# Kernel tuning notes

Hardware: AMD Instinct MI355X
Metric: run time of the kernel (lower is better)

## Reference

```python
import jax, jax.numpy as jnp
import numpy as np

B, C_IN, H, W = 4096, 3, 32, 32
C1, C2, K = 32, 64, 3
FC1, NCLS = 256, 10


def _extract_patches(x):
    # x: (B, C, H, W) -> patches (B, C, K*K, H, W), 3x3 neighborhoods, pad=1
    xp = jnp.pad(x, ((0, 0), (0, 0), (1, 1), (1, 1)))
    shifts = [xp[:, :, i:i + H, j:j + W] for i in range(K) for j in range(K)]
    return jnp.stack(shifts, axis=2)


def _maxpool2(x):
    b, c, h, w = x.shape
    return x.reshape(b, c, h // 2, 2, w // 2, 2).max(axis=(3, 5))


def setup_inputs() -> dict:
    key = jax.random.key(0)
    ks = jax.random.split(key, 9)
    # kaiming-ish scales
    s_lc = np.sqrt(2.0 / (C_IN * K * K)).astype(np.float32)
    s_cv = np.sqrt(2.0 / (C1 * K * K)).astype(np.float32)
    s_f1 = np.sqrt(2.0 / (C2 * 8 * 8)).astype(np.float32)
    s_f2 = np.sqrt(2.0 / FC1).astype(np.float32)
    return {
        "x": jax.random.normal(ks[0], (B, C_IN, H, W), dtype=jnp.float32),
        # unshared per-location weights: (O, C, K*K, H, W)
        "w_lc": jax.random.normal(ks[1], (C1, C_IN, K * K, H, W), dtype=jnp.float32) * s_lc,
        "b_lc": jnp.zeros((C1, H, W), dtype=jnp.float32),
        "w_conv": jax.random.normal(ks[2], (C2, C1, K, K), dtype=jnp.float32) * s_cv,
        "b_conv": jnp.zeros((C2,), dtype=jnp.float32),
        "w_fc1": jax.random.normal(ks[3], (FC1, C2 * 8 * 8), dtype=jnp.float32) * s_f1,
        "b_fc1": jnp.zeros((FC1,), dtype=jnp.float32),
        "w_fc2": jax.random.normal(ks[4], (NCLS, FC1), dtype=jnp.float32) * s_f2,
        "b_fc2": jnp.zeros((NCLS,), dtype=jnp.float32),
    }


def reference(x, w_lc, b_lc, w_conv, b_conv, w_fc1, b_fc1, w_fc2, b_fc2):
    # locally connected layer: per-(i,j) unshared 3x3 filters
    patches = _extract_patches(x)                                  # (B, C, 9, H, W)
    y = jnp.einsum('bckij,ockij->boij', patches, w_lc) + b_lc[None]  # (B, C1, H, W)
    y = jax.nn.relu(y)
    y = _maxpool2(y)                                               # (B, C1, 16, 16)
    # standard 3x3 conv, padding SAME
    y = jax.lax.conv_general_dilated(
        y, w_conv, window_strides=(1, 1), padding='SAME',
        dimension_numbers=('NCHW', 'OIHW', 'NCHW'))
    y = jax.nn.relu(y + b_conv[None, :, None, None])
    y = _maxpool2(y)                                               # (B, C2, 8, 8)
    y = y.reshape(y.shape[0], -1)                                  # (B, C2*8*8)
    y = jax.nn.relu(y @ w_fc1.T + b_fc1)
    return y @ w_fc2.T + b_fc2                                     # (B, num_classes)
```

## Files before the change

kernel.cpp:

```cpp
#include <hip/hip_runtime.h>

typedef short s16x8 __attribute__((ext_vector_type(8)));
typedef float f32x4 __attribute__((ext_vector_type(4)));
typedef unsigned short u16x4 __attribute__((ext_vector_type(4)));

static __device__ __forceinline__ unsigned short f2bf(float f) {
    union { float f; unsigned u; } v; v.f = f;
    unsigned r = v.u + 0x7FFF + ((v.u >> 16) & 1);
    return (unsigned short)(r >> 16);
}
static __device__ __forceinline__ float quad_fmax(float a) {
    int ai = __builtin_bit_cast(int, a);
    int s1 = __builtin_amdgcn_mov_dpp(ai, 0xB1, 0xF, 0xF, true);
    a = fmaxf(a, __builtin_bit_cast(float, s1));
    ai = __builtin_bit_cast(int, a);
    int s2 = __builtin_amdgcn_mov_dpp(ai, 0x4E, 0xF, 0xF, true);
    return fmaxf(a, __builtin_bit_cast(float, s2));
}

__global__ __launch_bounds__(256) void k_prep(
    const float* __restrict__ w_lc, const float* __restrict__ b_lc,
    const float* __restrict__ w_conv, const float* __restrict__ w_fc1,
    unsigned short* __restrict__ btab, unsigned short* __restrict__ wt_g,
    unsigned short* __restrict__ Wb)
{
    const int t = threadIdx.x, bx = blockIdx.x;
    if (bx < 1024) {
        const int gid = bx * 256 + t;
        const int k8 = gid & 7;
        const int nn = (gid >> 3) & 127;
        const int jp = (gid >> 10) & 15;
        const int pr = gid >> 14;
        const int o = nn >> 2, ih = (nn >> 1) & 1, jc = nn & 1;
        const int row = 2 * pr + ih, col = 2 * jp + jc;
        unsigned v32[8];
        #pragma unroll
        for (int e = 0; e < 8; ++e) {
            const int k = k8 * 8 + e;
            float v = 0.f;
            if (k < 48) {
                const int c = k >> 4, rr = (k >> 2) & 3, cf = k & 3;
                const int di = rr - ih, dj = cf - jc;
                if ((unsigned)di < 3u && (unsigned)dj < 3u)
                    v = w_lc[((o * 3 + c) * 9 + di * 3 + dj) * 1024 + row * 32 + col];
            } else if (k == 63) {
                v = b_lc[o * 1024 + row * 32 + col];
            }
            v32[e] = f2bf(v);
        }
        uint4 w;
        w.x = v32[0] | (v32[1] << 16);
        w.y = v32[2] | (v32[3] << 16);
        w.z = v32[4] | (v32[5] << 16);
        w.w = v32[6] | (v32[7] << 16);
        *(uint4*)&btab[(size_t)gid * 8] = w;
    } else if (bx < 1088) {
        const float4* wf4 = (const float4*)w_fc1;
        for (int f = t; f < 4096; f += 256) {
            const int idx = (bx - 1024) * 4096 + f;
            const float4 v = wf4[idx];
            u16x4 o = { f2bf(v.x), f2bf(v.y), f2bf(v.z), f2bf(v.w) };
            *(u16x4*)&Wb[idx * 4] = o;
        }
    } else {
        for (int i = t; i < 9 * 64 * 40; i += 256) wt_g[i] = 0;
        __syncthreads();
        for (int i = t; i < 64 * 32 * 9; i += 256) {
            const int oc = i / 288;
            const int rem = i - oc * 288;
            const int ic = rem / 9;
            const int kk = rem - ic * 9;
            wt_g[(kk * 64 + oc) * 40 + ic] = f2bf(w_conv[i]);
        }
    }
}

__global__ __launch_bounds__(256, 4) void k_lc(
    const float* __restrict__ x,
    const unsigned short* __restrict__ btab,
    unsigned short* __restrict__ y1g)
{
    __shared__ unsigned short xb_raw[8 + 12 * 33 * 34 + 8];
    __shared__ __align__(16) unsigned short pbuf[2][32][40];
    const int t = threadIdx.x;
    const int ib = blockIdx.x >> 4;
    const int pr = blockIdx.x & 15;
    const int img0 = ib * 32;
    unsigned short* xbp = xb_raw + 8;

    for (int f = t; f < (8 + 12 * 33 * 34 + 8) / 2; f += 256) ((int*)xb_raw)[f] = 0;
    __syncthreads();
    #pragma unroll
    for (int i = 0; i < 12; ++i) {
        const int f = t + i * 256;
        const int img = f / 96;
        const int rem = f - img * 96;
        const int c = rem >> 5, rr = (rem >> 3) & 3, cf = rem & 7;
        const int xrow = 2 * pr - 1 + rr;
        if ((unsigned)xrow < 32u) {
            const float4 v = *(const float4*)&x[
                ((size_t)(img0 + img) * 3 + c) * 1024 + xrow * 32 + cf * 4];
            const unsigned w0 = (unsigned)f2bf(v.x) | ((unsigned)f2bf(v.y) << 16);
            const unsigned w1 = (unsigned)f2bf(v.z) | ((unsigned)f2bf(v.w) << 16);
            const int imgl = (img & 15) + (img >> 4) * 17;
            const int sa = ((c * 4 + rr) * 33 + imgl) * 34 + cf * 4;
            *(unsigned*)&xbp[sa] = w0;
            *(unsigned*)&xbp[sa + 2] = w1;
        }
    }
    __syncthreads();

    const int lane = t & 63, wv = t >> 6;
    const int lc = lane & 15, lg = lane >> 4;
    const unsigned short* bpb = btab + (((size_t)pr * 16) * 128 + wv * 32) * 64;

    const int r1a = (8 + lg * 2 > 11) ? 11 : 8 + lg * 2;
    const int r1b = (9 + lg * 2 > 11) ? 11 : 9 + lg * 2;

#define LOADB(B, jpv)                                                          \
    {                                                                          \
        const unsigned short* bp = bpb + (size_t)(jpv) * (128 * 64);           \
        B[0] = *(const s16x8*)&bp[lc * 64 + lg * 8];                           \
        B[1] = *(const s16x8*)&bp[(16 + lc) * 64 + lg * 8];                    \
        B[2] = *(const s16x8*)&bp[lc * 64 + 32 + lg * 8];                      \
        B[3] = *(const s16x8*)&bp[(16 + lc) * 64 + 32 + lg * 8];               \
    }

#define ABUILD(wout, row0, row1, mbase, colb2, biasfix)                        \
    {                                                                          \
        const int rows_[2] = { row0, row1 };                                   \
        _Pragma("unroll")                                                      \
        for (int rI = 0; rI < 2; ++rI) {                                       \
            const int base = (rows_[rI] * 33 + (mbase)) * 34 + (colb2);        \
            const unsigned d0 = *(const unsigned*)&xbp[base];                  \
            const unsigned d1 = *(const unsigned*)&xbp[base + 2];              \
            const unsigned d2 = *(const unsigned*)&xbp[base + 4];              \
            wout[rI * 2 + 0] = (unsigned)(((((unsigned long long)d1) << 32) | d0) >> 16); \
            wout[rI * 2 + 1] = (unsigned)(((((unsigned long long)d2) << 32) | d1) >> 16); \
        }                                                                      \
        if (biasfix && lg == 3) wout[3] = 0x3F800000u;                         \
    }

#define STEP(jpv, B)                                                           \
    {                                                                          \
        const int colb2 = (jpv) * 2 - 2;                                       \
        f32x4 acc[2][2];                                                       \
        _Pragma("unroll")                                                      \
        for (int mh = 0; mh < 2; ++mh)                                         \
            _Pragma("unroll")                                                  \
            for (int nf = 0; nf < 2; ++nf) {                                   \
                f32x4 z = {0.f, 0.f, 0.f, 0.f};                                \
                acc[mh][nf] = z;                                               \
            }                                                                  \
        _Pragma("unroll")                                                      \
        for (int mh = 0; mh < 2; ++mh) {                                       \
            const int mbase = mh * 17 + lc;                                    \
            unsigned wa[4], wb[4];                                             \
            ABUILD(wa, lg * 2, lg * 2 + 1, mbase, colb2, 0)                    \
            ABUILD(wb, r1a, r1b, mbase, colb2, 1)                              \
            uint4 ai = { wa[0], wa[1], wa[2], wa[3] };                         \
            uint4 bi = { wb[0], wb[1], wb[2], wb[3] };                         \
            const s16x8 a0 = __builtin_bit_cast(s16x8, ai);                    \
            const s16x8 a1 = __builtin_bit_cast(s16x8, bi);                    \
            acc[mh][0] = __builtin_amdgcn_mfma_f32_16x16x32_bf16(a0, B[0], acc[mh][0], 0, 0, 0); \
            acc[mh][1] = __builtin_amdgcn_mfma_f32_16x16x32_bf16(a0, B[1], acc[mh][1], 0, 0, 0); \
            acc[mh][0] = __builtin_amdgcn_mfma_f32_16x16x32_bf16(a1, B[2], acc[mh][0], 0, 0, 0); \
            acc[mh][1] = __builtin_amdgcn_mfma_f32_16x16x32_bf16(a1, B[3], acc[mh][1], 0, 0, 0); \
        }                                                                      \
        _Pragma("unroll")                                                      \
        for (int mh = 0; mh < 2; ++mh)                                         \
            _Pragma("unroll")                                                  \
            for (int nf = 0; nf < 2; ++nf) {                                   \
                f32x4 v = acc[mh][nf];                                         \
                _Pragma("unroll")                                              \
                for (int q = 0; q < 4; ++q) v[q] = quad_fmax(v[q]);            \
                const float sel = (lc & 2) ? ((lc & 1) ? v[3] : v[2])          \
                                           : ((lc & 1) ? v[1] : v[0]);         \
                const float m = fmaxf(sel, 0.f);                               \
                pbuf[(jpv) & 1][mh * 16 + lg * 4 + (lc & 3)]                   \
                    [wv * 8 + nf * 4 + (lc >> 2)] = f2bf(m);                   \
            }                                                                  \
    }

    s16x8 Ba[4], Bb[4];
    LOADB(Ba, 0)
    for (int jp2 = 0; jp2 < 8; ++jp2) {
        LOADB(Bb, (jp2 * 2 + 1) & 15)
        STEP(jp2 * 2, Ba)
        LOADB(Ba, (jp2 * 2 + 2) & 15)
        STEP(jp2 * 2 + 1, Bb)
        {
            const int img = lane >> 1, jpq = lane & 1;
            const int jpg = jp2 * 2 + jpq;
            *(s16x8*)&y1g[(((size_t)(img0 + img) * 256) + pr * 16 + jpg) * 32 + wv * 8] =
                *(const s16x8*)&pbuf[jpq][img][wv * 8];
        }
    }
#undef STEP
#undef ABUILD
#undef LOADB
}

__global__ __launch_bounds__(256, 3) void k_conv(
    const unsigned short* __restrict__ y1g,
    const unsigned short* __restrict__ wt_g,
    const float* __restrict__ b_conv,
    unsigned short* __restrict__ p2)
{
    __shared__ __align__(16) unsigned short y1t[18][18][40];
    __shared__ __align__(16) unsigned short pbuf[4][1024];
    const int t = threadIdx.x;
    const int img = blockIdx.x;

    {
        const s16x8 z = {0, 0, 0, 0, 0, 0, 0, 0};
        unsigned short* p = &y1t[0][0][0];
        for (int i = t * 8; i < 18 * 18 * 40; i += 2048) *(s16x8*)(p + i) = z;
    }
    __syncthreads();
    {
        const int prr = t >> 4, pcc = t & 15;
        const unsigned short* src = y1g + ((size_t)img * 256 + t) * 32;
        unsigned short* d = &y1t[prr + 1][pcc + 1][0];
        #pragma unroll
        for (int ch = 0; ch < 4; ++ch)
            *(s16x8*)(d + ch * 8) = *(const s16x8*)(src + ch * 8);
    }
    __syncthreads();

    const int w = t >> 6, lane = t & 63;
    const int lc = lane & 15, lg = lane >> 4;

    f32x4 acc[4][4];
    #pragma unroll
    for (int mf = 0; mf < 4; ++mf)
        #pragma unroll
        for (int nf = 0; nf < 4; ++nf) {
            f32x4 zz = {0.f, 0.f, 0.f, 0.f};
            acc[mf][nf] = zz;
        }
    #pragma unroll
    for (int kk = 0; kk < 9; ++kk) {
        const int di = kk / 3, dj = kk % 3;
        s16x8 a[4], bb[4];
        #pragma unroll
        for (int nf = 0; nf < 4; ++nf)
            bb[nf] = *(const s16x8*)&wt_g[(kk * 64 + nf * 16 + lc) * 40 + lg * 8];
        #pragma unroll
        for (int mf = 0; mf < 4; ++mf)
            a[mf] = *(const s16x8*)&y1t[w * 4 + mf + di][lc + dj][lg * 8];
        #pragma unroll
        for (int mf = 0; mf < 4; ++mf)
            #pragma unroll
            for (int nf = 0; nf < 4; ++nf)
                acc[mf][nf] = __builtin_amdgcn_mfma_f32_16x16x32_bf16(
                    a[mf], bb[nf], acc[mf][nf], 0, 0, 0);
    }
    #pragma unroll
    for (int mfp = 0; mfp < 2; ++mfp) {
        #pragma unroll
        for (int nf = 0; nf < 4; ++nf) {
            const f32x4 u = acc[mfp * 2][nf], v = acc[mfp * 2 + 1][nf];
            const float bbv = b_conv[nf * 16 + lc];
            float q0 = fmaxf(fmaxf(u[0], u[1]), fmaxf(v[0], v[1]));
            float q1 = fmaxf(fmaxf(u[2], u[3]), fmaxf(v[2], v[3]));
            q0 = fmaxf(q0 + bbv, 0.f);
            q1 = fmaxf(q1 + bbv, 0.f);
            *(unsigned*)&pbuf[w][(nf * 16 + lc) * 16 + mfp * 8 + lg * 2] =
                (unsigned)f2bf(q0) | ((unsigned)f2bf(q1) << 16);
        }
    }
    #pragma unroll
    for (int jj = 0; jj < 2; ++jj) {
        const int u8 = jj * 64 + lane;
        const int oc = u8 >> 1, s = (u8 & 1) * 8;
        const s16x8 val = *(const s16x8*)&pbuf[w][u8 * 8];
        *(s16x8*)&p2[((size_t)img * 64 + oc) * 64 + w * 16 + s] = val;
    }
}

__global__ __launch_bounds__(256) void k_fc1(
    const unsigned short* __restrict__ A,
    const unsigned short* __restrict__ Wb,
    const float* __restrict__ bias, float* __restrict__ fc1p)
{
    __shared__ __align__(16) unsigned short As[64][72];
    __shared__ __align__(16) unsigned short Bs[32][72];
    const int t = threadIdx.x;
    const int m0 = blockIdx.x * 64, n0 = blockIdx.y * 32;
    const int z = blockIdx.z;
    const int w = t >> 6, lane = t & 63;
    const int lc = lane & 15, lg = lane >> 4;
    f32x4 acc[2];
    {
        const float bv0 = (z == 0) ? bias[n0 + lc] : 0.f;
        const float bv1 = (z == 0) ? bias[n0 + 16 + lc] : 0.f;
        f32x4 a0 = {bv0, bv0, bv0, bv0}, a1 = {bv1, bv1, bv1, bv1};
        acc[0] = a0; acc[1] = a1;
    }
    const int kbase = z * 2048;
    for (int k0 = kbase; k0 < kbase + 2048; k0 += 64) {
        {
            const int r0 = t >> 3, ch0 = (t & 7) * 8;
            const int id1 = t + 256;
            const int r1 = id1 >> 3, ch1 = (id1 & 7) * 8;
            *(s16x8*)&As[r0][ch0] = *(const s16x8*)&A[(size_t)(m0 + r0) * 4096 + k0 + ch0];
            *(s16x8*)&As[r1][ch1] = *(const s16x8*)&A[(size_t)(m0 + r1) * 4096 + k0 + ch1];
            const int rb = t >> 3, cb = (t & 7) * 8;
            *(s16x8*)&Bs[rb][cb] = *(const s16x8*)&Wb[(size_t)(n0 + rb) * 4096 + k0 + cb];
        }
        __syncthreads();
        #pragma unroll
        for (int kh = 0; kh < 2; ++kh) {
            const s16x8 a  = *(const s16x8*)&As[w * 16 + lc][kh * 32 + lg * 8];
            const s16x8 b0 = *(const s16x8*)&Bs[lc][kh * 32 + lg * 8];
            const s16x8 b1 = *(const s16x8*)&Bs[16 + lc][kh * 32 + lg * 8];
            acc[0] = __builtin_amdgcn_mfma_f32_16x16x32_bf16(a, b0, acc[0], 0, 0, 0);
            acc[1] = __builtin_amdgcn_mfma_f32_16x16x32_bf16(a, b1, acc[1], 0, 0, 0);
        }
        __syncthreads();
    }
    #pragma unroll
    for (int nf = 0; nf < 2; ++nf) {
        const int n = n0 + nf * 16 + lc;
        #pragma unroll
        for (int q = 0; q < 4; ++q) {
            const int m = m0 + w * 16 + lg * 4 + q;
            fc1p[((size_t)z * 4096 + m) * 256 + n] = acc[nf][q];
        }
    }
}

__global__ __launch_bounds__(320) void k_fc2(
    const float* __restrict__ fc1p, const float* __restrict__ Wt,
    const float* __restrict__ bias, float* __restrict__ out)
{
    const int t = threadIdx.x;
    const int r = blockIdx.x * 32 + t / 10;
    const int n = t % 10;
    const float4* a0 = (const float4*)(fc1p + (size_t)r * 256);
    const float4* a1 = (const float4*)(fc1p + (size_t)(4096 + r) * 256);
    const float4* w = (const float4*)(Wt + (size_t)n * 256);
    float acc = bias[n];
    #pragma unroll 8
    for (int k = 0; k < 64; ++k) {
        const float4 u = a0[k], v = a1[k], wv = w[k];
        acc += fmaxf(u.x + v.x, 0.f) * wv.x + fmaxf(u.y + v.y, 0.f) * wv.y +
               fmaxf(u.z + v.z, 0.f) * wv.z + fmaxf(u.w + v.w, 0.f) * wv.w;
    }
    out[(size_t)r * 10 + n] = acc;
}

extern "C" void kernel_launch(void* const* d_in, const int* in_sizes, int n_in,
                              void* d_out, int out_size, void* d_ws, size_t ws_size,
                              hipStream_t stream)
{
    const float* x      = (const float*)d_in[0];
    const float* w_lc   = (const float*)d_in[1];
    const float* b_lc   = (const float*)d_in[2];
    const float* w_conv = (const float*)d_in[3];
    const float* b_conv = (const float*)d_in[4];
    const float* w_fc1  = (const float*)d_in[5];
    const float* b_fc1  = (const float*)d_in[6];
    const float* w_fc2  = (const float*)d_in[7];
    const float* b_fc2  = (const float*)d_in[8];
    float* out = (float*)d_out;

    unsigned short* p2b  = (unsigned short*)d_ws;
    unsigned short* btab = (unsigned short*)((char*)d_ws + 16777216);
    unsigned short* y1g  = (unsigned short*)((char*)d_ws + 33554432);
    float*          fc1p = (float*)((char*)d_ws + 33554432);
    unsigned short* Wb   = (unsigned short*)((char*)d_ws + 67108864);
    unsigned short* wt_g = (unsigned short*)((char*)d_ws + 69206016);

    k_prep<<<1089, 256, 0, stream>>>(w_lc, b_lc, w_conv, w_fc1, btab, wt_g, Wb);
    for (int half = 0; half < 2; ++half) {
        k_lc<<<1024, 256, 0, stream>>>(x + (size_t)half * 2048 * 3072, btab, y1g);
        k_conv<<<2048, 256, 0, stream>>>(y1g, wt_g, b_conv,
                                         p2b + (size_t)half * 2048 * 4096);
    }
    k_fc1<<<dim3(64, 8, 2), 256, 0, stream>>>(p2b, Wb, b_fc1, fc1p);
    k_fc2<<<128, 320, 0, stream>>>(fc1p, w_fc2, b_fc2, out);
}
```

Baseline: 200.3 us.

## Halve images per locally-connected block to raise occupancy and simplify loop

Each k_lc block now processes 16 images instead of 32, and the grid doubles to 2048 blocks. This halves the shared-memory input tile and pooled buffer, and the launch bound allows 8 blocks per CU instead of 4. The explicit double-buffered prefetch of the B fragments is replaced by a plain per-column loop with one M-tile. Each wave now stores its pooled outputs directly from a single buffer through its first 16 lanes. In exchange, per-location weights are reloaded twice as often across the grid, and without the software prefetch the compiler must hide the load latency.

```diff
diff --git a/kernel.cpp b/kernel.cpp
--- a/kernel.cpp
+++ b/kernel.cpp
@@ -75,23 +75,23 @@
     }
 }
 
-__global__ __launch_bounds__(256, 4) void k_lc(
+__global__ __launch_bounds__(256, 8) void k_lc(
     const float* __restrict__ x,
     const unsigned short* __restrict__ btab,
     unsigned short* __restrict__ y1g)
 {
-    __shared__ unsigned short xb_raw[8 + 12 * 33 * 34 + 8];
-    __shared__ __align__(16) unsigned short pbuf[2][32][40];
+    __shared__ unsigned short xb_raw[8 + 12 * 17 * 34 + 8];
+    __shared__ __align__(16) unsigned short pbuf[16][40];
     const int t = threadIdx.x;
     const int ib = blockIdx.x >> 4;
     const int pr = blockIdx.x & 15;
-    const int img0 = ib * 32;
+    const int img0 = ib * 16;
     unsigned short* xbp = xb_raw + 8;
 
-    for (int f = t; f < (8 + 12 * 33 * 34 + 8) / 2; f += 256) ((int*)xb_raw)[f] = 0;
+    for (int f = t; f < (8 + 12 * 17 * 34 + 8) / 2; f += 256) ((int*)xb_raw)[f] = 0;
     __syncthreads();
     #pragma unroll
-    for (int i = 0; i < 12; ++i) {
+    for (int i = 0; i < 6; ++i) {
         const int f = t + i * 256;
         const int img = f / 96;
         const int rem = f - img * 96;
@@ -102,8 +102,7 @@
                 ((size_t)(img0 + img) * 3 + c) * 1024 + xrow * 32 + cf * 4];
             const unsigned w0 = (unsigned)f2bf(v.x) | ((unsigned)f2bf(v.y) << 16);
             const unsigned w1 = (unsigned)f2bf(v.z) | ((unsigned)f2bf(v.w) << 16);
-            const int imgl = (img & 15) + (img >> 4) * 17;
-            const int sa = ((c * 4 + rr) * 33 + imgl) * 34 + cf * 4;
+            const int sa = ((c * 4 + rr) * 17 + img) * 34 + cf * 4;
             *(unsigned*)&xbp[sa] = w0;
             *(unsigned*)&xbp[sa + 2] = w1;
         }
@@ -117,21 +116,14 @@
     const int r1a = (8 + lg * 2 > 11) ? 11 : 8 + lg * 2;
     const int r1b = (9 + lg * 2 > 11) ? 11 : 9 + lg * 2;
 
-#define LOADB(B, jpv)                                                          \
-    {                                                                          \
-        const unsigned short* bp = bpb + (size_t)(jpv) * (128 * 64);           \
-        B[0] = *(const s16x8*)&bp[lc * 64 + lg * 8];                           \
-        B[1] = *(const s16x8*)&bp[(16 + lc) * 64 + lg * 8];                    \
-        B[2] = *(const s16x8*)&bp[lc * 64 + 32 + lg * 8];                      \
-        B[3] = *(const s16x8*)&bp[(16 + lc) * 64 + 32 + lg * 8];               \
-    }
-
-#define ABUILD(wout, row0, row1, mbase, colb2, biasfix)                        \
+    unsigned short* ybase = y1g + (((size_t)(img0 + lc) * 256) + pr * 16) * 32 + wv * 8;
+
+#define ABUILD(wout, row0, row1, colb2, biasfix)                               \
     {                                                                          \
         const int rows_[2] = { row0, row1 };                                   \
         _Pragma("unroll")                                                      \
         for (int rI = 0; rI < 2; ++rI) {                                       \
-            const int base = (rows_[rI] * 33 + (mbase)) * 34 + (colb2);        \
+            const int base = (rows_[rI] * 17 + lc) * 34 + (colb2);             \
             const unsigned d0 = *(const unsigned*)&xbp[base];                  \
             const unsigned d1 = *(const unsigned*)&xbp[base + 2];              \
             const unsigned d2 = *(const unsigned*)&xbp[base + 4];              \
@@ -141,64 +133,47 @@
         if (biasfix && lg == 3) wout[3] = 0x3F800000u;                         \
     }
 
-#define STEP(jpv, B)                                                           \
-    {                                                                          \
-        const int colb2 = (jpv) * 2 - 2;                                       \
-        f32x4 acc[2][2];                                                       \
-        _Pragma("unroll")                                                      \
-        for (int mh = 0; mh < 2; ++mh)                                         \
-            _Pragma("unroll")                                                  \
-            for (int nf = 0; nf < 2; ++nf) {                                   \
-                f32x4 z = {0.f, 0.f, 0.f, 0.f};                                \
-                acc[mh][nf] = z;                                               \
-            }                                                                  \
-        _Pragma("unroll")                                                      \
-        for (int mh = 0; mh < 2; ++mh) {                                       \
-            const int mbase = mh * 17 + lc;                                    \
-            unsigned wa[4], wb[4];                                             \
-            ABUILD(wa, lg * 2, lg * 2 + 1, mbase, colb2, 0)                    \
-            ABUILD(wb, r1a, r1b, mbase, colb2, 1)                              \
-            uint4 ai = { wa[0], wa[1], wa[2], wa[3] };                         \
-            uint4 bi = { wb[0], wb[1], wb[2], wb[3] };                         \
-            const s16x8 a0 = __builtin_bit_cast(s16x8, ai);                    \
-            const s16x8 a1 = __builtin_bit_cast(s16x8, bi);                    \
-            acc[mh][0] = __builtin_amdgcn_mfma_f32_16x16x32_bf16(a0, B[0], acc[mh][0], 0, 0, 0); \
-            acc[mh][1] = __builtin_amdgcn_mfma_f32_16x16x32_bf16(a0, B[1], acc[mh][1], 0, 0, 0); \
-            acc[mh][0] = __builtin_amdgcn_mfma_f32_16x16x32_bf16(a1, B[2], acc[mh][0], 0, 0, 0); \
-            acc[mh][1] = __builtin_amdgcn_mfma_f32_16x16x32_bf16(a1, B[3], acc[mh][1], 0, 0, 0); \
-        }                                                                      \
-        _Pragma("unroll")                                                      \
-        for (int mh = 0; mh < 2; ++mh)                                         \
-            _Pragma("unroll")                                                  \
-            for (int nf = 0; nf < 2; ++nf) {                                   \
-                f32x4 v = acc[mh][nf];                                         \
-                _Pragma("unroll")                                              \
-                for (int q = 0; q < 4; ++q) v[q] = quad_fmax(v[q]);            \
-                const float sel = (lc & 2) ? ((lc & 1) ? v[3] : v[2])          \
-                                           : ((lc & 1) ? v[1] : v[0]);         \
-                const float m = fmaxf(sel, 0.f);                               \
-                pbuf[(jpv) & 1][mh * 16 + lg * 4 + (lc & 3)]                   \
-                    [wv * 8 + nf * 4 + (lc >> 2)] = f2bf(m);                   \
-            }                                                                  \
-    }
-
-    s16x8 Ba[4], Bb[4];
-    LOADB(Ba, 0)
-    for (int jp2 = 0; jp2 < 8; ++jp2) {
-        LOADB(Bb, (jp2 * 2 + 1) & 15)
-        STEP(jp2 * 2, Ba)
-        LOADB(Ba, (jp2 * 2 + 2) & 15)
-        STEP(jp2 * 2 + 1, Bb)
+    for (int jp = 0; jp < 16; ++jp) {
+        const int colb2 = jp * 2 - 2;
+        const unsigned short* bp = bpb + (size_t)jp * (128 * 64);
+        const s16x8 B0 = *(const s16x8*)&bp[lc * 64 + lg * 8];
+        const s16x8 B1 = *(const s16x8*)&bp[(16 + lc) * 64 + lg * 8];
+        const s16x8 B2 = *(const s16x8*)&bp[lc * 64 + 32 + lg * 8];
+        const s16x8 B3 = *(const s16x8*)&bp[(16 + lc) * 64 + 32 + lg * 8];
+
+        unsigned wa[4], wb[4];
+        ABUILD(wa, lg * 2, lg * 2 + 1, colb2, 0)
+        ABUILD(wb, r1a, r1b, colb2, 1)
+        uint4 ai = { wa[0], wa[1], wa[2], wa[3] };
+        uint4 bi = { wb[0], wb[1], wb[2], wb[3] };
+        const s16x8 a0 = __builtin_bit_cast(s16x8, ai);
+        const s16x8 a1 = __builtin_bit_cast(s16x8, bi);
+
+        f32x4 acc[2];
         {
-            const int img = lane >> 1, jpq = lane & 1;
-            const int jpg = jp2 * 2 + jpq;
-            *(s16x8*)&y1g[(((size_t)(img0 + img) * 256) + pr * 16 + jpg) * 32 + wv * 8] =
-                *(const s16x8*)&pbuf[jpq][img][wv * 8];
-        }
-    }
-#undef STEP
+            f32x4 z = {0.f, 0.f, 0.f, 0.f};
+            acc[0] = z; acc[1] = z;
+        }
+        acc[0] = __builtin_amdgcn_mfma_f32_16x16x32_bf16(a0, B0, acc[0], 0, 0, 0);
+        acc[1] = __builtin_amdgcn_mfma_f32_16x16x32_bf16(a0, B1, acc[1], 0, 0, 0);
+        acc[0] = __builtin_amdgcn_mfma_f32_16x16x32_bf16(a1, B2, acc[0], 0, 0, 0);
+        acc[1] = __builtin_amdgcn_mfma_f32_16x16x32_bf16(a1, B3, acc[1], 0, 0, 0);
+
+        #pragma unroll
+        for (int nf = 0; nf < 2; ++nf) {
+            f32x4 v = acc[nf];
+            #pragma unroll
+            for (int q = 0; q < 4; ++q) v[q] = quad_fmax(v[q]);
+            const float sel = (lc & 2) ? ((lc & 1) ? v[3] : v[2])
+                                       : ((lc & 1) ? v[1] : v[0]);
+            const float m = fmaxf(sel, 0.f);
+            pbuf[lg * 4 + (lc & 3)][wv * 8 + nf * 4 + (lc >> 2)] = f2bf(m);
+        }
+        if (lg == 0) {
+            *(s16x8*)&ybase[(size_t)jp * 32] = *(const s16x8*)&pbuf[lc][wv * 8];
+        }
+    }
 #undef ABUILD
-#undef LOADB
 }
 
 __global__ __launch_bounds__(256, 3) void k_conv(
@@ -375,7 +350,7 @@
 
     k_prep<<<1089, 256, 0, stream>>>(w_lc, b_lc, w_conv, w_fc1, btab, wt_g, Wb);
     for (int half = 0; half < 2; ++half) {
-        k_lc<<<1024, 256, 0, stream>>>(x + (size_t)half * 2048 * 3072, btab, y1g);
+        k_lc<<<2048, 256, 0, stream>>>(x + (size_t)half * 2048 * 3072, btab, y1g);
         k_conv<<<2048, 256, 0, stream>>>(y1g, wt_g, b_conv,
                                          p2b + (size_t)half * 2048 * 4096);
     }
```

New measurement: 246.8 us. 1.23x slower.
